# Kernel optimization log

Measured on AMD Instinct MI355X. Metric: run time of the kernel, lower is better.

## Reference

```python
import jax, jax.numpy as jnp
import numpy as np


def setup_inputs() -> dict:
    key = jax.random.key(0)
    kx, kb, kc, ka, kd = jax.random.split(key, 5)
    B, L, D, N = 8, 4096, 1024, 128
    x = jax.random.normal(kx, (B, L, D), jnp.float32)
    B_w = jax.random.normal(kb, (N, D), jnp.float32) * 0.01  # nn.Linear(d_model->d_state).weight
    C_w = jax.random.normal(kc, (D, N), jnp.float32)         # nn.Linear(d_state->d_model).weight
    # stable negative log_A (HiPPO init gives -|diag|+0.1 < 0)
    log_A = -jax.random.uniform(ka, (N,), jnp.float32) * 3.0 - 0.1
    D_param = jax.random.normal(kd, (D,), jnp.float32)
    return dict(x=x, B_w=B_w, C_w=C_w, log_A=log_A, D_param=D_param)


def reference(x, B_w, C_w, log_A, D_param):
    # x: (B,L,D); B_w: (N,D); C_w: (D,N); log_A: (N,); D_param: (D,)
    A = jnp.exp(log_A)                                   # (N,) diagonal transition
    x_proj = jnp.einsum('bld,nd->bln', x, B_w)           # B @ x  -> (B,L,N)

    def step(h, u):                                      # h_t = A*h_{t-1} + u_t
        h = A * h + u
        return h, h

    h0 = jnp.zeros((x.shape[0], B_w.shape[0]), x.dtype)  # (B,N)
    _, hs = jax.lax.scan(step, h0, jnp.swapaxes(x_proj, 0, 1))  # hs: (L,B,N)

    y = jnp.einsum('lbn,dn->bld', hs, C_w)               # C @ h -> (B,L,D)
    y = y + x * D_param                                  # skip term D*x

    last = x_proj[:, -1, :]                              # (B,N)
    final_state = jnp.broadcast_to(last.mean(axis=0, keepdims=True), last.shape)
    return y, final_state
```

## Files before the change

kernel.cpp:

```cpp
#include <hip/hip_runtime.h>


typedef _Float16 half8 __attribute__((ext_vector_type(8)));
typedef _Float16 half4 __attribute__((ext_vector_type(4)));
typedef float f32x4 __attribute__((ext_vector_type(4)));

#define BDIM 8
#define LDIM 4096
#define DDIM 1024
#define NDIM 128
#define MTOT (BDIM * LDIM)
#define CHUNK 32
#define NCHUNK (LDIM / CHUNK)
#define TOTCHUNK (BDIM * NCHUNK)

__global__ __launch_bounds__(256) void prep(const float* __restrict__ x,
                                            const float* __restrict__ Bw,
                                            const float* __restrict__ Cw,
                                            _Float16* __restrict__ Bwh,
                                            _Float16* __restrict__ Cwh,
                                            float* __restrict__ out) {
    const int blk = blockIdx.x;
    const int t = threadIdx.x;
    if (blk < 128) {
        const int n = blk;
        float s = 0.f;
        const float* br = Bw + n * DDIM;
        for (int b = 0; b < BDIM; ++b) {
            const float* xr = x + ((size_t)b * LDIM + (LDIM - 1)) * DDIM;
            for (int k = t; k < DDIM; k += 256)
                s = fmaf(xr[k], br[k], s);
        }
        __shared__ float red[256];
        red[t] = s;
        __syncthreads();
        for (int off = 128; off > 0; off >>= 1) {
            if (t < off) red[t] += red[t + off];
            __syncthreads();
        }
        if (t == 0) {
            float v = red[0] * 0.125f;
            for (int b = 0; b < BDIM; ++b)
                out[(size_t)MTOT * DDIM + b * NDIM + n] = v;
        }
    } else {
        const int base = (blk - 128) * 4096;
#pragma unroll
        for (int j = 0; j < 4; ++j) {
            int e = base + j * 1024 + t * 4;
            const float* src;
            _Float16* dst;
            if (e < 131072) { src = Bw + e; dst = Bwh + e; }
            else            { src = Cw + (e - 131072); dst = Cwh + (e - 131072); }
            float4 v = *reinterpret_cast<const float4*>(src);
            half4 h = { (_Float16)v.x, (_Float16)v.y, (_Float16)v.z, (_Float16)v.w };
            *reinterpret_cast<half4*>(dst) = h;
        }
    }
}

__global__ __launch_bounds__(256) void gemm1(const float* __restrict__ x,
                                             const _Float16* __restrict__ Bwh,
                                             float* __restrict__ xp) {
    const int t = threadIdx.x;
    const int row0 = blockIdx.x * 64;
    const int wave = t >> 6, lane = t & 63;
    const int wr = (wave >> 1) * 32, wc = (wave & 1) * 64;
    const int lrow = lane & 15, kq = (lane >> 4) * 8;

    f32x4 acc[2][4] = {};
    const float* a0 = x + (size_t)(row0 + wr + lrow) * DDIM + kq;
    const float* a1 = a0 + 16 * DDIM;
    const _Float16* b0 = Bwh + (size_t)(wc + lrow) * DDIM + kq;

    for (int kk = 0; kk < DDIM; kk += 32) {
        half8 bf[4];
#pragma unroll
        for (int ct = 0; ct < 4; ++ct)
            bf[ct] = *reinterpret_cast<const half8*>(b0 + (size_t)ct * 16 * DDIM + kk);
        half8 af[2];
#pragma unroll
        for (int rt = 0; rt < 2; ++rt) {
            const float* ap = (rt ? a1 : a0) + kk;
            float4 v0 = *reinterpret_cast<const float4*>(ap);
            float4 v1 = *reinterpret_cast<const float4*>(ap + 4);
            af[rt] = half8{ (_Float16)v0.x, (_Float16)v0.y, (_Float16)v0.z, (_Float16)v0.w,
                            (_Float16)v1.x, (_Float16)v1.y, (_Float16)v1.z, (_Float16)v1.w };
        }
#pragma unroll
        for (int rt = 0; rt < 2; ++rt)
#pragma unroll
            for (int ct = 0; ct < 4; ++ct)
                acc[rt][ct] = __builtin_amdgcn_mfma_f32_16x16x32_f16(af[rt], bf[ct], acc[rt][ct], 0, 0, 0);
    }

    const int q4 = (lane >> 4) * 4;
#pragma unroll
    for (int rt = 0; rt < 2; ++rt)
#pragma unroll
        for (int ct = 0; ct < 4; ++ct) {
            int col = wc + ct * 16 + lrow;
#pragma unroll
            for (int i = 0; i < 4; ++i)
                xp[(row0 + wr + rt * 16 + q4 + i) * NDIM + col] = acc[rt][ct][i];
        }
}

__global__ void scan_agg(const float* __restrict__ xp, const float* __restrict__ logA,
                         float* __restrict__ agg) {
    const int chunk = blockIdx.x;
    const int n = threadIdx.x;
    const float A = expf(logA[n]);
    const float* u = xp + (size_t)chunk * CHUNK * NDIM + n;
    float h = 0.f;
#pragma unroll
    for (int j = 0; j < CHUNK; ++j)
        h = fmaf(A, h, u[j * NDIM]);
    agg[chunk * NDIM + n] = h;
}

__global__ void scan_carry(const float* __restrict__ agg, const float* __restrict__ logA,
                           float* __restrict__ hprev) {
    const int idx = blockIdx.x * blockDim.x + threadIdx.x;
    const int b = idx >> 7, n = idx & 127;
    const float Ac = expf((float)CHUNK * logA[n]);
    float c = 0.f;
    for (int ch = 0; ch < NCHUNK; ++ch) {
        int g = (b * NCHUNK + ch) * NDIM + n;
        hprev[g] = c;
        c = fmaf(Ac, c, agg[g]);
    }
}

__global__ void scan_final(const float* __restrict__ xp, const float* __restrict__ logA,
                           const float* __restrict__ hprev, _Float16* __restrict__ hs) {
    const int chunk = blockIdx.x;
    const int n = threadIdx.x;
    const float A = expf(logA[n]);
    float h = hprev[chunk * NDIM + n];
    const float* u = xp + (size_t)chunk * CHUNK * NDIM + n;
    _Float16* o = hs + (size_t)chunk * CHUNK * NDIM + n;
#pragma unroll
    for (int j = 0; j < CHUNK; ++j) {
        h = fmaf(A, h, u[j * NDIM]);
        o[j * NDIM] = (_Float16)h;
    }
}

#define BUFW 132
__global__ __launch_bounds__(256, 4) void gemm2(const _Float16* __restrict__ hs,
                                                const _Float16* __restrict__ Cwh,
                                                const float* __restrict__ x,
                                                const float* __restrict__ Dp,
                                                float* __restrict__ y) {
    __shared__ float buf[64 * BUFW];
    __shared__ __align__(16) float DpS[128];

    const int t = threadIdx.x;
    const int row0 = blockIdx.x * 128;
    const int col0 = blockIdx.y * 128;
    const int wave = t >> 6, lane = t & 63;
    const int wr = (wave >> 1) * 64, wc = (wave & 1) * 64;
    const int lrow = lane & 15, kq = (lane >> 4) * 8;

    if (t < 128) DpS[t] = Dp[col0 + t];

    const _Float16* ha = hs + (size_t)(row0 + wr + lrow) * NDIM + kq;
    const _Float16* cb = Cwh + (size_t)(col0 + wc + lrow) * NDIM + kq;

    f32x4 acc[4][4] = {};
#pragma unroll
    for (int kb = 0; kb < 4; ++kb) {
        half8 bf[4], af[4];
#pragma unroll
        for (int ct = 0; ct < 4; ++ct)
            bf[ct] = *reinterpret_cast<const half8*>(cb + (size_t)ct * 16 * NDIM + kb * 32);
#pragma unroll
        for (int rt = 0; rt < 4; ++rt)
            af[rt] = *reinterpret_cast<const half8*>(ha + (size_t)rt * 16 * NDIM + kb * 32);
#pragma unroll
        for (int rt = 0; rt < 4; ++rt)
#pragma unroll
            for (int ct = 0; ct < 4; ++ct)
                acc[rt][ct] = __builtin_amdgcn_mfma_f32_16x16x32_f16(af[rt], bf[ct], acc[rt][ct], 0, 0, 0);
    }

    const int q4 = (lane >> 4) * 4;
#pragma unroll
    for (int half_ = 0; half_ < 2; ++half_) {
        __syncthreads();
        if ((wr >> 6) == half_) {
#pragma unroll
            for (int rt = 0; rt < 4; ++rt)
#pragma unroll
                for (int ct = 0; ct < 4; ++ct) {
                    int col = wc + ct * 16 + lrow;
#pragma unroll
                    for (int i = 0; i < 4; ++i)
                        buf[(rt * 16 + q4 + i) * BUFW + col] = acc[rt][ct][i];
                }
        }
        __syncthreads();
#pragma unroll
        for (int j = 0; j < 8; ++j) {
            int idx = t + 256 * j;
            int row = idx >> 5, c4 = idx & 31;
            int grow = row0 + half_ * 64 + row;
            float4 a = *reinterpret_cast<const float4*>(&buf[row * BUFW + c4 * 4]);
            float4 xv = *reinterpret_cast<const float4*>(&x[(size_t)grow * DDIM + col0 + c4 * 4]);
            float4 dp = *reinterpret_cast<const float4*>(&DpS[c4 * 4]);
            float4 o;
            o.x = a.x + xv.x * dp.x;
            o.y = a.y + xv.y * dp.y;
            o.z = a.z + xv.z * dp.z;
            o.w = a.w + xv.w * dp.w;
            *reinterpret_cast<float4*>(&y[(size_t)grow * DDIM + col0 + c4 * 4]) = o;
        }
    }
}

extern "C" void kernel_launch(void* const* d_in, const int* in_sizes, int n_in,
                              void* d_out, int out_size, void* d_ws, size_t ws_size,
                              hipStream_t stream) {
    const float* x    = (const float*)d_in[0];
    const float* Bw   = (const float*)d_in[1];
    const float* Cw   = (const float*)d_in[2];
    const float* logA = (const float*)d_in[3];
    const float* Dp   = (const float*)d_in[4];
    float* out = (float*)d_out;

    char* ws = (char*)d_ws;
    float*    xp    = (float*)   (ws);
    _Float16* hs    = (_Float16*)(ws + 16777216);
    float*    agg   = (float*)   (ws + 25165824);
    float*    hprev = (float*)   (ws + 25690112);
    _Float16* Bwh   = (_Float16*)(ws + 26214400);
    _Float16* Cwh   = (_Float16*)(ws + 26476544);

    prep<<<192, 256, 0, stream>>>(x, Bw, Cw, Bwh, Cwh, out);
    gemm1<<<MTOT / 64, 256, 0, stream>>>(x, Bwh, xp);
    scan_agg<<<TOTCHUNK, 128, 0, stream>>>(xp, logA, agg);
    scan_carry<<<4, 256, 0, stream>>>(agg, logA, hprev);
    scan_final<<<TOTCHUNK, 128, 0, stream>>>(xp, logA, hprev, hs);
    gemm2<<<dim3(MTOT / 128, DDIM / 128), 256, 0, stream>>>(hs, Cwh, x, Dp, out);
}
```

Baseline: 361.7 us.

## Stage gemm1 tiles in LDS with async global-to-LDS loads and XOR swizzle

Rewrites the first projection GEMM to stage the fp16 B_w tile into shared memory via global_load_lds DMA and the converted x tile via regular stores, both with an XOR swizzle to avoid bank conflicts. The block row tile shrinks from 64 to 32 rows with more blocks and an occupancy hint of 4 blocks per CU. This aims to replace uncoalesced per-lane global fragment loads with coalesced tile loads, at the cost of two barriers per k-step and more reloads of B_w per row.

```diff
diff --git a/kernel.cpp b/kernel.cpp
--- a/kernel.cpp
+++ b/kernel.cpp
@@ -13,6 +13,11 @@
 #define CHUNK 32
 #define NCHUNK (LDIM / CHUNK)
 #define TOTCHUNK (BDIM * NCHUNK)
+
+__device__ __forceinline__ void dma16(const void* g, void* l) {
+    __builtin_amdgcn_global_load_lds((const __attribute__((address_space(1))) void*)g,
+                                     (__attribute__((address_space(3))) void*)l, 16, 0, 0);
+}
 
 __global__ __launch_bounds__(256) void prep(const float* __restrict__ x,
                                             const float* __restrict__ Bw,
@@ -59,51 +64,66 @@
     }
 }
 
-__global__ __launch_bounds__(256) void gemm1(const float* __restrict__ x,
-                                             const _Float16* __restrict__ Bwh,
-                                             float* __restrict__ xp) {
+__global__ __launch_bounds__(256, 4) void gemm1(const float* __restrict__ x,
+                                                const _Float16* __restrict__ Bwh,
+                                                float* __restrict__ xp) {
+    __shared__ _Float16 As[32 * 64];
+    __shared__ _Float16 Bs[128 * 64];
     const int t = threadIdx.x;
-    const int row0 = blockIdx.x * 64;
+    const int row0 = blockIdx.x * 32;
     const int wave = t >> 6, lane = t & 63;
-    const int wr = (wave >> 1) * 32, wc = (wave & 1) * 64;
+    const int wr = (wave >> 1) * 16, wc = (wave & 1) * 64;
     const int lrow = lane & 15, kq = (lane >> 4) * 8;
-
-    f32x4 acc[2][4] = {};
-    const float* a0 = x + (size_t)(row0 + wr + lrow) * DDIM + kq;
-    const float* a1 = a0 + 16 * DDIM;
-    const _Float16* b0 = Bwh + (size_t)(wc + lrow) * DDIM + kq;
-
-    for (int kk = 0; kk < DDIM; kk += 32) {
-        half8 bf[4];
-#pragma unroll
-        for (int ct = 0; ct < 4; ++ct)
-            bf[ct] = *reinterpret_cast<const half8*>(b0 + (size_t)ct * 16 * DDIM + kk);
-        half8 af[2];
-#pragma unroll
-        for (int rt = 0; rt < 2; ++rt) {
-            const float* ap = (rt ? a1 : a0) + kk;
-            float4 v0 = *reinterpret_cast<const float4*>(ap);
-            float4 v1 = *reinterpret_cast<const float4*>(ap + 4);
-            af[rt] = half8{ (_Float16)v0.x, (_Float16)v0.y, (_Float16)v0.z, (_Float16)v0.w,
-                            (_Float16)v1.x, (_Float16)v1.y, (_Float16)v1.z, (_Float16)v1.w };
-        }
-#pragma unroll
-        for (int rt = 0; rt < 2; ++rt)
+    const int kc = kq >> 3;
+
+    f32x4 acc[4] = {};
+
+    for (int kk = 0; kk < DDIM; kk += 64) {
+#pragma unroll
+        for (int inst = 0; inst < 4; ++inst) {
+            int s = inst * 256 + t;
+            int r = s >> 3;
+            int cs = (s & 7) ^ (r & 7);
+            dma16(&Bwh[(size_t)r * DDIM + kk + cs * 8], &Bs[(inst * 256 + wave * 64) * 8]);
+        }
+#pragma unroll
+        for (int j = 0; j < 2; ++j) {
+            int s = t + 256 * j;
+            int r = s >> 4, c4 = s & 15;
+            float4 v = *reinterpret_cast<const float4*>(&x[(size_t)(row0 + r) * DDIM + kk + c4 * 4]);
+            half4 h = { (_Float16)v.x, (_Float16)v.y, (_Float16)v.z, (_Float16)v.w };
+            int pc = (c4 >> 1) ^ (r & 7);
+            *reinterpret_cast<half4*>(&As[r * 64 + pc * 8 + (c4 & 1) * 4]) = h;
+        }
+        __syncthreads();
+
+        half8 af[2], bf[2][4];
+        const int arow = wr + lrow;
+#pragma unroll
+        for (int ks = 0; ks < 2; ++ks) {
+            af[ks] = *reinterpret_cast<const half8*>(&As[arow * 64 + ((ks * 4 + kc) ^ (arow & 7)) * 8]);
+#pragma unroll
+            for (int ct = 0; ct < 4; ++ct) {
+                int brow = wc + ct * 16 + lrow;
+                bf[ks][ct] = *reinterpret_cast<const half8*>(&Bs[brow * 64 + ((ks * 4 + kc) ^ (brow & 7)) * 8]);
+            }
+        }
+#pragma unroll
+        for (int ks = 0; ks < 2; ++ks)
 #pragma unroll
             for (int ct = 0; ct < 4; ++ct)
-                acc[rt][ct] = __builtin_amdgcn_mfma_f32_16x16x32_f16(af[rt], bf[ct], acc[rt][ct], 0, 0, 0);
+                acc[ct] = __builtin_amdgcn_mfma_f32_16x16x32_f16(af[ks], bf[ks][ct], acc[ct], 0, 0, 0);
+        __syncthreads();
     }
 
     const int q4 = (lane >> 4) * 4;
 #pragma unroll
-    for (int rt = 0; rt < 2; ++rt)
-#pragma unroll
-        for (int ct = 0; ct < 4; ++ct) {
-            int col = wc + ct * 16 + lrow;
-#pragma unroll
-            for (int i = 0; i < 4; ++i)
-                xp[(row0 + wr + rt * 16 + q4 + i) * NDIM + col] = acc[rt][ct][i];
-        }
+    for (int ct = 0; ct < 4; ++ct) {
+        int col = wc + ct * 16 + lrow;
+#pragma unroll
+        for (int i = 0; i < 4; ++i)
+            xp[(row0 + wr + q4 + i) * NDIM + col] = acc[ct][i];
+    }
 }
 
 __global__ void scan_agg(const float* __restrict__ xp, const float* __restrict__ logA,
@@ -238,7 +258,7 @@
     _Float16* Cwh   = (_Float16*)(ws + 26476544);
 
     prep<<<192, 256, 0, stream>>>(x, Bw, Cw, Bwh, Cwh, out);
-    gemm1<<<MTOT / 64, 256, 0, stream>>>(x, Bwh, xp);
+    gemm1<<<MTOT / 32, 256, 0, stream>>>(x, Bwh, xp);
     scan_agg<<<TOTCHUNK, 128, 0, stream>>>(xp, logA, agg);
     scan_carry<<<4, 256, 0, stream>>>(agg, logA, hprev);
     scan_final<<<TOTCHUNK, 128, 0, stream>>>(xp, logA, hprev, hs);
```

After: 343.6 us. 5.0% less time.
